# Kernel optimization log

Hardware: AMD Instinct MI355X
Metric: run time of the kernel (lower is better)

## Reference

```python
import jax, jax.numpy as jnp
import numpy as np


def setup_inputs() -> dict:
    key = jax.random.key(0)
    k1, k2, k3, k4, k5 = jax.random.split(key, 5)
    B, S, D, U = 64, 2048, 512, 512
    he = lambda k, shape: jax.random.normal(k, shape, dtype=jnp.float32) * jnp.sqrt(2.0 / shape[0])
    return {
        "query": jax.random.normal(k1, (B, D), dtype=jnp.float32),
        "values": jax.random.normal(k2, (B, S, D), dtype=jnp.float32),
        "W1": he(k3, (D, U)),
        "W2": he(k4, (D, U)),
        "V1": he(k5, (U, 1)),
    }


def reference(query, values, W1, W2, V1):
    # query: (B, D), values: (B, S, D)
    Q = query @ W1                       # (B, U)
    V = jnp.einsum("bsd,du->bsu", values, W2)  # (B, S, U)
    add = jnp.tanh(Q[:, None, :] + V)    # (B, S, U)
    score = jnp.einsum("bsu,uo->bso", add, V1)  # (B, S, 1)
    attn = jax.nn.softmax(score, axis=1)         # (B, S, 1)
    context = jnp.sum(attn * values, axis=1)     # (B, D)
    return context
```

## Files before the change

kernel.cpp:

```cpp
#include <hip/hip_runtime.h>


typedef __attribute__((ext_vector_type(8))) short bf16x8;
typedef __attribute__((ext_vector_type(4))) float f32x4;

#if __has_builtin(__builtin_amdgcn_exp2f)
__device__ __forceinline__ float fast_exp2(float x) { return __builtin_amdgcn_exp2f(x); }
#else
__device__ __forceinline__ float fast_exp2(float x) { return exp2f(x); }
#endif
#if __has_builtin(__builtin_amdgcn_rcpf)
__device__ __forceinline__ float fast_rcp(float x) { return __builtin_amdgcn_rcpf(x); }
#else
__device__ __forceinline__ float fast_rcp(float x) { return 1.0f / x; }
#endif

__device__ __forceinline__ unsigned short f2bf(float f) {
  unsigned int u = __float_as_uint(f);
  u += 0x7fffu + ((u >> 16) & 1u);
  return (unsigned short)(u >> 16);
}

__global__ void qk(const float* __restrict__ query, const float* __restrict__ W1,
                   float* __restrict__ Q) {
  __shared__ float qrow[512];
  const int b = blockIdx.x, half = blockIdx.y, t = threadIdx.x;
  qrow[t] = query[b * 512 + t];
  qrow[t + 256] = query[b * 512 + t + 256];
  __syncthreads();
  const int u = half * 256 + t;
  float acc = 0.f;
#pragma unroll 8
  for (int k = 0; k < 512; ++k) acc += qrow[k] * W1[(size_t)k * 512 + u];
  Q[b * 512 + u] = acc;
}

__global__ void wt_k(const float* __restrict__ W2, unsigned short* __restrict__ Wtf,
                     float* __restrict__ out0) {
  const int gid = blockIdx.x * 256 + threadIdx.x;
  out0[gid] = 0.f;
  const int lane = gid & 63;
  const int g = gid >> 6;
  const int ks = g & 15, ntile = g >> 4;
  const int l15 = lane & 15, quad = lane >> 4;
  const int n = ntile * 16 + l15;
  const int k0 = ks * 32 + quad * 8;
  unsigned int p[4];
#pragma unroll
  for (int jj = 0; jj < 4; ++jj) {
    const float a = W2[(size_t)(k0 + 2 * jj) * 512 + n];
    const float b = W2[(size_t)(k0 + 2 * jj + 1) * 512 + n];
    p[jj] = (unsigned int)f2bf(a) | ((unsigned int)f2bf(b) << 16);
  }
  *(uint4*)&Wtf[(size_t)gid * 8] = make_uint4(p[0], p[1], p[2], p[3]);
}

__global__ __launch_bounds__(512, 4) void scores_k(
    const float* __restrict__ values, const unsigned short* __restrict__ Wtf,
    const float* __restrict__ Q, const float* __restrict__ V1,
    float* __restrict__ scores) {
  __shared__ __align__(16) unsigned short Ab[64 * 512];
  __shared__ float sAcc[64];

  const int t = threadIdx.x;
  const int lane = t & 63;
  const int w = t >> 6;
  const int quad = lane >> 4;
  const int l15 = lane & 15;
  const int m0 = blockIdx.x * 64;
  const int b = m0 >> 11;

  if (t < 64) sAcc[t] = 0.0f;

  const float* Ag = values + (size_t)m0 * 512;
#pragma unroll
  for (int i = 0; i < 8; ++i) {
    const int c = i * 512 + t;
    const int m = c >> 6;
    const int kc = c & 63;
    const float4* src = (const float4*)(Ag + (size_t)m * 512 + kc * 8);
    const float4 x = src[0], y = src[1];
    const unsigned int p0 = (unsigned int)f2bf(x.x) | ((unsigned int)f2bf(x.y) << 16);
    const unsigned int p1 = (unsigned int)f2bf(x.z) | ((unsigned int)f2bf(x.w) << 16);
    const unsigned int p2 = (unsigned int)f2bf(y.x) | ((unsigned int)f2bf(y.y) << 16);
    const unsigned int p3 = (unsigned int)f2bf(y.z) | ((unsigned int)f2bf(y.w) << 16);
    *(uint4*)&Ab[m * 512 + ((kc ^ (m & 7)) * 8)] = make_uint4(p0, p1, p2, p3);
  }
  __syncthreads();

  f32x4 acc[4][4];
#pragma unroll
  for (int mt = 0; mt < 4; ++mt)
#pragma unroll
    for (int nt = 0; nt < 4; ++nt) acc[mt][nt] = (f32x4){0.f, 0.f, 0.f, 0.f};

  const unsigned short* Bg = Wtf + (size_t)lane * 8;
  const int sw = l15 & 7;

#pragma unroll
  for (int ks = 0; ks < 16; ++ks) {
    bf16x8 bfr[4], af[4];
#pragma unroll
    for (int nt = 0; nt < 4; ++nt)
      bfr[nt] = *(const bf16x8*)(Bg + (size_t)((w * 4 + nt) * 16 + ks) * 512);
#pragma unroll
    for (int mt = 0; mt < 4; ++mt) {
      const int m = mt * 16 + l15;
      af[mt] = *(const bf16x8*)&Ab[m * 512 + (((ks * 4 + quad) ^ sw) * 8)];
    }
#pragma unroll
    for (int mt = 0; mt < 4; ++mt)
#pragma unroll
      for (int nt = 0; nt < 4; ++nt)
        acc[mt][nt] = __builtin_amdgcn_mfma_f32_16x16x32_bf16(af[mt], bfr[nt],
                                                              acc[mt][nt], 0, 0, 0);
  }

  float part[4][4];
#pragma unroll
  for (int mt = 0; mt < 4; ++mt)
#pragma unroll
    for (int r = 0; r < 4; ++r) part[mt][r] = 0.f;

#pragma unroll
  for (int nt = 0; nt < 4; ++nt) {
    const int n = w * 64 + nt * 16 + l15;
    const float qv = Q[b * 512 + n];
    const float v1 = V1[n];
#pragma unroll
    for (int mt = 0; mt < 4; ++mt)
#pragma unroll
      for (int r = 0; r < 4; ++r) {
        const float x = acc[mt][nt][r] + qv;
        const float e = fast_exp2(x * 2.8853900817779268f);
        const float th = 1.0f - 2.0f * fast_rcp(e + 1.0f);
        part[mt][r] += th * v1;
      }
  }
#pragma unroll
  for (int mt = 0; mt < 4; ++mt)
#pragma unroll
    for (int r = 0; r < 4; ++r) {
      float v = part[mt][r];
      v += __shfl_xor(v, 1);
      v += __shfl_xor(v, 2);
      v += __shfl_xor(v, 4);
      v += __shfl_xor(v, 8);
      if (l15 == 0) atomicAdd(&sAcc[mt * 16 + quad * 4 + r], v);
    }
  __syncthreads();
  if (t < 64) scores[m0 + t] = sAcc[t];
}

__global__ __launch_bounds__(512) void ctx_k(const float* __restrict__ values,
                                             const float* __restrict__ scores,
                                             float* __restrict__ out) {
  __shared__ float red[16];
  __shared__ float wsc[256];
  const int bid = blockIdx.x;
  const int b = bid >> 3, sc = bid & 7;
  const int t = threadIdx.x;
  const float* sb = scores + (size_t)b * 2048;
  const float v0 = sb[t], v1 = sb[t + 512], v2 = sb[t + 1024], v3 = sb[t + 1536];
  float mx = fmaxf(fmaxf(v0, v1), fmaxf(v2, v3));
#pragma unroll
  for (int o = 1; o < 64; o <<= 1) mx = fmaxf(mx, __shfl_xor(mx, o));
  if ((t & 63) == 0) red[t >> 6] = mx;
  __syncthreads();
  mx = fmaxf(fmaxf(fmaxf(red[0], red[1]), fmaxf(red[2], red[3])),
             fmaxf(fmaxf(red[4], red[5]), fmaxf(red[6], red[7])));
  const float L2E = 1.4426950408889634f;
  float sum = fast_exp2((v0 - mx) * L2E) + fast_exp2((v1 - mx) * L2E) +
              fast_exp2((v2 - mx) * L2E) + fast_exp2((v3 - mx) * L2E);
#pragma unroll
  for (int o = 1; o < 64; o <<= 1) sum += __shfl_xor(sum, o);
  if ((t & 63) == 0) red[8 + (t >> 6)] = sum;
  __syncthreads();
  sum = (red[8] + red[9]) + (red[10] + red[11]) + (red[12] + red[13]) +
        (red[14] + red[15]);
  const float inv = 1.0f / sum;
  if (t < 256) wsc[t] = fast_exp2((sb[sc * 256 + t] - mx) * L2E) * inv;
  __syncthreads();
  const float* vb = values + ((size_t)b * 2048 + sc * 256) * 512;
  float acc = 0.f;
#pragma unroll 8
  for (int s = 0; s < 256; ++s) acc += wsc[s] * vb[(size_t)s * 512 + t];
  atomicAdd(&out[b * 512 + t], acc);
}

extern "C" void kernel_launch(void* const* d_in, const int* in_sizes, int n_in,
                              void* d_out, int out_size, void* d_ws, size_t ws_size,
                              hipStream_t stream) {
  const float* query = (const float*)d_in[0];
  const float* values = (const float*)d_in[1];
  const float* W1 = (const float*)d_in[2];
  const float* W2 = (const float*)d_in[3];
  const float* V1 = (const float*)d_in[4];
  float* out = (float*)d_out;

  char* ws = (char*)d_ws;
  float* Qp = (float*)ws;
  unsigned short* Wtp = (unsigned short*)(ws + 131072);
  float* Sp = (float*)(ws + 131072 + 524288);

  qk<<<dim3(64, 2), 256, 0, stream>>>(query, W1, Qp);
  wt_k<<<128, 256, 0, stream>>>(W2, Wtp, out);
  scores_k<<<2048, 512, 0, stream>>>(values, Wtp, Qp, V1, Sp);
  ctx_k<<<512, 512, 0, stream>>>(values, Sp, out);
}
```

Measured before the change: 499.7 us.

## Double-buffer K-chunks of values in scores kernel; split context kernel finer

The scores kernel no longer stages the full 64x512 bf16 tile of values before any MFMA work. It splits K into four 128-wide chunks in a double-buffered LDS tile, prefetching the next chunk's fp32 loads into registers while MFMAs run on the current chunk. This cuts LDS use per block, which can allow more resident blocks, and overlaps global loads with compute, at the cost of extra barriers. The context kernel also doubles its grid to 1024 blocks, each handling 128 sequence positions, for more parallelism at the cost of more atomics and repeated softmax reductions.

```diff
diff --git a/kernel.cpp b/kernel.cpp
--- a/kernel.cpp
+++ b/kernel.cpp
@@ -59,7 +59,7 @@
     const float* __restrict__ values, const unsigned short* __restrict__ Wtf,
     const float* __restrict__ Q, const float* __restrict__ V1,
     float* __restrict__ scores) {
-  __shared__ __align__(16) unsigned short Ab[64 * 512];
+  __shared__ __align__(16) unsigned short Ab[2][64 * 128];
   __shared__ float sAcc[64];
 
   const int t = threadIdx.x;
@@ -72,19 +72,26 @@
 
   if (t < 64) sAcc[t] = 0.0f;
 
-  const float* Ag = values + (size_t)m0 * 512;
-#pragma unroll
-  for (int i = 0; i < 8; ++i) {
-    const int c = i * 512 + t;
-    const int m = c >> 6;
-    const int kc = c & 63;
-    const float4* src = (const float4*)(Ag + (size_t)m * 512 + kc * 8);
-    const float4 x = src[0], y = src[1];
-    const unsigned int p0 = (unsigned int)f2bf(x.x) | ((unsigned int)f2bf(x.y) << 16);
-    const unsigned int p1 = (unsigned int)f2bf(x.z) | ((unsigned int)f2bf(x.w) << 16);
-    const unsigned int p2 = (unsigned int)f2bf(y.x) | ((unsigned int)f2bf(y.y) << 16);
-    const unsigned int p3 = (unsigned int)f2bf(y.z) | ((unsigned int)f2bf(y.w) << 16);
-    *(uint4*)&Ab[m * 512 + ((kc ^ (m & 7)) * 8)] = make_uint4(p0, p1, p2, p3);
+  const int sm = t >> 3;
+  const int sp = t & 7;
+  const int sk = sm & 7;
+  const float* src = values + (size_t)(m0 + sm) * 512 + sp * 16;
+  const int wo0 = sm * 128 + (((2 * sp) ^ sk) * 8);
+  const int wo1 = sm * 128 + (((2 * sp + 1) ^ sk) * 8);
+
+  {
+    const f32x4* s4 = (const f32x4*)src;
+    const f32x4 r0 = s4[0], r1 = s4[1], r2 = s4[2], r3 = s4[3];
+    const unsigned int p0 = (unsigned int)f2bf(r0[0]) | ((unsigned int)f2bf(r0[1]) << 16);
+    const unsigned int p1 = (unsigned int)f2bf(r0[2]) | ((unsigned int)f2bf(r0[3]) << 16);
+    const unsigned int p2 = (unsigned int)f2bf(r1[0]) | ((unsigned int)f2bf(r1[1]) << 16);
+    const unsigned int p3 = (unsigned int)f2bf(r1[2]) | ((unsigned int)f2bf(r1[3]) << 16);
+    const unsigned int p4 = (unsigned int)f2bf(r2[0]) | ((unsigned int)f2bf(r2[1]) << 16);
+    const unsigned int p5 = (unsigned int)f2bf(r2[2]) | ((unsigned int)f2bf(r2[3]) << 16);
+    const unsigned int p6 = (unsigned int)f2bf(r3[0]) | ((unsigned int)f2bf(r3[1]) << 16);
+    const unsigned int p7 = (unsigned int)f2bf(r3[2]) | ((unsigned int)f2bf(r3[3]) << 16);
+    *(uint4*)&Ab[0][wo0] = make_uint4(p0, p1, p2, p3);
+    *(uint4*)&Ab[0][wo1] = make_uint4(p4, p5, p6, p7);
   }
   __syncthreads();
 
@@ -98,22 +105,49 @@
   const int sw = l15 & 7;
 
 #pragma unroll
-  for (int ks = 0; ks < 16; ++ks) {
-    bf16x8 bfr[4], af[4];
-#pragma unroll
-    for (int nt = 0; nt < 4; ++nt)
-      bfr[nt] = *(const bf16x8*)(Bg + (size_t)((w * 4 + nt) * 16 + ks) * 512);
-#pragma unroll
-    for (int mt = 0; mt < 4; ++mt) {
-      const int m = mt * 16 + l15;
-      af[mt] = *(const bf16x8*)&Ab[m * 512 + (((ks * 4 + quad) ^ sw) * 8)];
-    }
-#pragma unroll
-    for (int mt = 0; mt < 4; ++mt)
+  for (int c = 0; c < 4; ++c) {
+    f32x4 r0, r1, r2, r3;
+    if (c < 3) {
+      const f32x4* s4 = (const f32x4*)(src + (c + 1) * 128);
+      r0 = s4[0];
+      r1 = s4[1];
+      r2 = s4[2];
+      r3 = s4[3];
+      asm volatile("" : "+v"(r0), "+v"(r1), "+v"(r2), "+v"(r3));
+    }
+
+    const unsigned short* Ac = &Ab[c & 1][0];
+#pragma unroll
+    for (int kl = 0; kl < 4; ++kl) {
+      const int ks = c * 4 + kl;
+      bf16x8 bfr[4], af[4];
 #pragma unroll
       for (int nt = 0; nt < 4; ++nt)
-        acc[mt][nt] = __builtin_amdgcn_mfma_f32_16x16x32_bf16(af[mt], bfr[nt],
-                                                              acc[mt][nt], 0, 0, 0);
+        bfr[nt] = *(const bf16x8*)(Bg + (size_t)((w * 4 + nt) * 16 + ks) * 512);
+#pragma unroll
+      for (int mt = 0; mt < 4; ++mt)
+        af[mt] = *(const bf16x8*)&Ac[(mt * 16 + l15) * 128 + (((kl * 4 + quad) ^ sw) * 8)];
+#pragma unroll
+      for (int mt = 0; mt < 4; ++mt)
+#pragma unroll
+        for (int nt = 0; nt < 4; ++nt)
+          acc[mt][nt] = __builtin_amdgcn_mfma_f32_16x16x32_bf16(af[mt], bfr[nt],
+                                                                acc[mt][nt], 0, 0, 0);
+    }
+
+    if (c < 3) {
+      const unsigned int p0 = (unsigned int)f2bf(r0[0]) | ((unsigned int)f2bf(r0[1]) << 16);
+      const unsigned int p1 = (unsigned int)f2bf(r0[2]) | ((unsigned int)f2bf(r0[3]) << 16);
+      const unsigned int p2 = (unsigned int)f2bf(r1[0]) | ((unsigned int)f2bf(r1[1]) << 16);
+      const unsigned int p3 = (unsigned int)f2bf(r1[2]) | ((unsigned int)f2bf(r1[3]) << 16);
+      const unsigned int p4 = (unsigned int)f2bf(r2[0]) | ((unsigned int)f2bf(r2[1]) << 16);
+      const unsigned int p5 = (unsigned int)f2bf(r2[2]) | ((unsigned int)f2bf(r2[3]) << 16);
+      const unsigned int p6 = (unsigned int)f2bf(r3[0]) | ((unsigned int)f2bf(r3[1]) << 16);
+      const unsigned int p7 = (unsigned int)f2bf(r3[2]) | ((unsigned int)f2bf(r3[3]) << 16);
+      *(uint4*)&Ab[(c + 1) & 1][wo0] = make_uint4(p0, p1, p2, p3);
+      *(uint4*)&Ab[(c + 1) & 1][wo1] = make_uint4(p4, p5, p6, p7);
+    }
+    __syncthreads();
   }
 
   float part[4][4];
@@ -156,9 +190,9 @@
                                              const float* __restrict__ scores,
                                              float* __restrict__ out) {
   __shared__ float red[16];
-  __shared__ float wsc[256];
+  __shared__ float wsc[128];
   const int bid = blockIdx.x;
-  const int b = bid >> 3, sc = bid & 7;
+  const int b = bid >> 4, sc = bid & 15;
   const int t = threadIdx.x;
   const float* sb = scores + (size_t)b * 2048;
   const float v0 = sb[t], v1 = sb[t + 512], v2 = sb[t + 1024], v3 = sb[t + 1536];
@@ -179,12 +213,12 @@
   sum = (red[8] + red[9]) + (red[10] + red[11]) + (red[12] + red[13]) +
         (red[14] + red[15]);
   const float inv = 1.0f / sum;
-  if (t < 256) wsc[t] = fast_exp2((sb[sc * 256 + t] - mx) * L2E) * inv;
-  __syncthreads();
-  const float* vb = values + ((size_t)b * 2048 + sc * 256) * 512;
+  if (t < 128) wsc[t] = fast_exp2((sb[sc * 128 + t] - mx) * L2E) * inv;
+  __syncthreads();
+  const float* vb = values + ((size_t)b * 2048 + sc * 128) * 512;
   float acc = 0.f;
 #pragma unroll 8
-  for (int s = 0; s < 256; ++s) acc += wsc[s] * vb[(size_t)s * 512 + t];
+  for (int s = 0; s < 128; ++s) acc += wsc[s] * vb[(size_t)s * 512 + t];
   atomicAdd(&out[b * 512 + t], acc);
 }
 
@@ -206,5 +240,5 @@
   qk<<<dim3(64, 2), 256, 0, stream>>>(query, W1, Qp);
   wt_k<<<128, 256, 0, stream>>>(W2, Wtp, out);
   scores_k<<<2048, 512, 0, stream>>>(values, Wtp, Qp, V1, Sp);
-  ctx_k<<<512, 512, 0, stream>>>(values, Sp, out);
-}
+  ctx_k<<<1024, 512, 0, stream>>>(values, Sp, out);
+}
```

Measured after the change: 505.4 us. No clear change (+1.1%).

## Fuse softmax-weighted context into score kernel with split-softmax partial combine

Applied to the files above, without the earlier changes.

Each score block now computes a local max and exp-sum over its 64 rows and immediately accumulates a partial context from those same values rows while they are likely still cache-resident. A small combine kernel then rescales the 32 partials per batch with an online-softmax correction. The aim is to avoid the second full read of the 256 MB values tensor in the old ctx kernel, as well as the output atomics. The cost is a 4 MB partial-context buffer and extra per-block work after the MFMA phase.

```diff
diff --git a/kernel.cpp b/kernel.cpp
--- a/kernel.cpp
+++ b/kernel.cpp
@@ -35,10 +35,8 @@
   Q[b * 512 + u] = acc;
 }
 
-__global__ void wt_k(const float* __restrict__ W2, unsigned short* __restrict__ Wtf,
-                     float* __restrict__ out0) {
+__global__ void wt_k(const float* __restrict__ W2, unsigned short* __restrict__ Wtf) {
   const int gid = blockIdx.x * 256 + threadIdx.x;
-  out0[gid] = 0.f;
   const int lane = gid & 63;
   const int g = gid >> 6;
   const int ks = g & 15, ntile = g >> 4;
@@ -55,19 +53,21 @@
   *(uint4*)&Wtf[(size_t)gid * 8] = make_uint4(p[0], p[1], p[2], p[3]);
 }
 
-__global__ __launch_bounds__(512, 4) void scores_k(
+__global__ __launch_bounds__(512, 4) void scorectx_k(
     const float* __restrict__ values, const unsigned short* __restrict__ Wtf,
     const float* __restrict__ Q, const float* __restrict__ V1,
-    float* __restrict__ scores) {
+    float* __restrict__ Pstat, float* __restrict__ Pctx) {
   __shared__ __align__(16) unsigned short Ab[64 * 512];
   __shared__ float sAcc[64];
+  __shared__ float wLDS[64];
 
   const int t = threadIdx.x;
   const int lane = t & 63;
   const int w = t >> 6;
   const int quad = lane >> 4;
   const int l15 = lane & 15;
-  const int m0 = blockIdx.x * 64;
+  const int blk = blockIdx.x;
+  const int m0 = blk * 64;
   const int b = m0 >> 11;
 
   if (t < 64) sAcc[t] = 0.0f;
@@ -149,43 +149,57 @@
       if (l15 == 0) atomicAdd(&sAcc[mt * 16 + quad * 4 + r], v);
     }
   __syncthreads();
-  if (t < 64) scores[m0 + t] = sAcc[t];
-}
-
-__global__ __launch_bounds__(512) void ctx_k(const float* __restrict__ values,
-                                             const float* __restrict__ scores,
-                                             float* __restrict__ out) {
-  __shared__ float red[16];
-  __shared__ float wsc[256];
-  const int bid = blockIdx.x;
-  const int b = bid >> 3, sc = bid & 7;
-  const int t = threadIdx.x;
-  const float* sb = scores + (size_t)b * 2048;
-  const float v0 = sb[t], v1 = sb[t + 512], v2 = sb[t + 1024], v3 = sb[t + 1536];
-  float mx = fmaxf(fmaxf(v0, v1), fmaxf(v2, v3));
-#pragma unroll
-  for (int o = 1; o < 64; o <<= 1) mx = fmaxf(mx, __shfl_xor(mx, o));
-  if ((t & 63) == 0) red[t >> 6] = mx;
-  __syncthreads();
-  mx = fmaxf(fmaxf(fmaxf(red[0], red[1]), fmaxf(red[2], red[3])),
-             fmaxf(fmaxf(red[4], red[5]), fmaxf(red[6], red[7])));
+
   const float L2E = 1.4426950408889634f;
-  float sum = fast_exp2((v0 - mx) * L2E) + fast_exp2((v1 - mx) * L2E) +
-              fast_exp2((v2 - mx) * L2E) + fast_exp2((v3 - mx) * L2E);
-#pragma unroll
-  for (int o = 1; o < 64; o <<= 1) sum += __shfl_xor(sum, o);
-  if ((t & 63) == 0) red[8 + (t >> 6)] = sum;
-  __syncthreads();
-  sum = (red[8] + red[9]) + (red[10] + red[11]) + (red[12] + red[13]) +
-        (red[14] + red[15]);
-  const float inv = 1.0f / sum;
-  if (t < 256) wsc[t] = fast_exp2((sb[sc * 256 + t] - mx) * L2E) * inv;
-  __syncthreads();
-  const float* vb = values + ((size_t)b * 2048 + sc * 256) * 512;
+  if (t < 64) {
+    const float v = sAcc[t];
+    float m = v;
+#pragma unroll
+    for (int o = 1; o < 64; o <<= 1) m = fmaxf(m, __shfl_xor(m, o));
+    const float wv = fast_exp2((v - m) * L2E);
+    float dsum = wv;
+#pragma unroll
+    for (int o = 1; o < 64; o <<= 1) dsum += __shfl_xor(dsum, o);
+    wLDS[t] = wv;
+    if (t == 0) {
+      Pstat[2 * blk] = m;
+      Pstat[2 * blk + 1] = dsum;
+    }
+  }
+  __syncthreads();
+
+  const float* vrow = values + (size_t)m0 * 512 + t;
+  float cacc = 0.f;
+#pragma unroll 8
+  for (int r = 0; r < 64; ++r) cacc += wLDS[r] * vrow[(size_t)r * 512];
+  Pctx[(size_t)blk * 512 + t] = cacc;
+}
+
+__global__ __launch_bounds__(512) void comb_k(const float* __restrict__ Pstat,
+                                              const float* __restrict__ Pctx,
+                                              float* __restrict__ out) {
+  __shared__ float aL[32];
+  __shared__ float Dsh;
+  const int b = blockIdx.x, t = threadIdx.x;
+  const float L2E = 1.4426950408889634f;
+  if (t < 32) {
+    const float2 st = ((const float2*)Pstat)[b * 32 + t];
+    float m = st.x;
+#pragma unroll
+    for (int o = 1; o < 32; o <<= 1) m = fmaxf(m, __shfl_xor(m, o));
+    const float a = fast_exp2((st.x - m) * L2E);
+    float D = a * st.y;
+#pragma unroll
+    for (int o = 1; o < 32; o <<= 1) D += __shfl_xor(D, o);
+    aL[t] = a;
+    if (t == 0) Dsh = D;
+  }
+  __syncthreads();
+  const float* pc = Pctx + (size_t)b * 32 * 512 + t;
   float acc = 0.f;
-#pragma unroll 8
-  for (int s = 0; s < 256; ++s) acc += wsc[s] * vb[(size_t)s * 512 + t];
-  atomicAdd(&out[b * 512 + t], acc);
+#pragma unroll
+  for (int i = 0; i < 32; ++i) acc += aL[i] * pc[(size_t)i * 512];
+  out[b * 512 + t] = acc / Dsh;
 }
 
 extern "C" void kernel_launch(void* const* d_in, const int* in_sizes, int n_in,
@@ -201,10 +215,11 @@
   char* ws = (char*)d_ws;
   float* Qp = (float*)ws;
   unsigned short* Wtp = (unsigned short*)(ws + 131072);
-  float* Sp = (float*)(ws + 131072 + 524288);
+  float* Pstat = (float*)(ws + 131072 + 524288);
+  float* Pctx = (float*)(ws + 131072 + 524288 + 16384);
 
   qk<<<dim3(64, 2), 256, 0, stream>>>(query, W1, Qp);
-  wt_k<<<128, 256, 0, stream>>>(W2, Wtp, out);
-  scores_k<<<2048, 512, 0, stream>>>(values, Wtp, Qp, V1, Sp);
-  ctx_k<<<512, 512, 0, stream>>>(values, Sp, out);
-}
+  wt_k<<<128, 256, 0, stream>>>(W2, Wtp);
+  scorectx_k<<<2048, 512, 0, stream>>>(values, Wtp, Qp, V1, Pstat, Pctx);
+  comb_k<<<64, 512, 0, stream>>>(Pstat, Pctx, out);
+}
```

Result: faster. 477.3 us (-4.5%).
